# Performance work log

Hardware: AMD Instinct MI355X
Metric: run time of the kernel (lower is better)

## Reference

```python
import jax, jax.numpy as jnp
import numpy as np


def setup_inputs() -> dict:
    key = jax.random.key(0)
    ks = jax.random.split(key, 5)
    B, IN, OUT = 8192, 4096, 4096
    in_q, out_q = IN // 4, OUT // 4
    # xavier-uniform-like scale for weights
    lim = float(np.sqrt(6.0 / (in_q + out_q)))
    return {
        "x": jax.random.normal(ks[0], (B, IN), dtype=jnp.float32),
        "Wa": jax.random.uniform(ks[1], (in_q, out_q), jnp.float32, -lim, lim),
        "Wb": jax.random.uniform(ks[2], (in_q, out_q), jnp.float32, -lim, lim),
        "Wc": jax.random.uniform(ks[3], (in_q, out_q), jnp.float32, -lim, lim),
        "Wd": jax.random.uniform(ks[4], (in_q, out_q), jnp.float32, -lim, lim),
        "bias": jnp.zeros((OUT,), dtype=jnp.float32),
    }


def reference(x, Wa, Wb, Wc, Wd, bias):
    # split quaternion components: [B, in_q] each
    a, b, c, d = jnp.split(x, 4, axis=1)
    # Hamilton product with weight quaternion (right multiplication)
    out_a = a @ Wa - b @ Wb - c @ Wc - d @ Wd
    out_b = a @ Wb + b @ Wa + c @ Wd - d @ Wc
    out_c = a @ Wc - b @ Wd + c @ Wa + d @ Wb
    out_d = a @ Wd + b @ Wc - c @ Wb + d @ Wa
    return jnp.concatenate([out_a, out_b, out_c, out_d], axis=1) + bias
```

## Files before the change

kernel.cpp:

```cpp
#include <hip/hip_runtime.h>
#include <hip/hip_bf16.h>
#include <cstdint>
#include <cstddef>

typedef __bf16 bf16_t;
typedef __bf16 bf16x4 __attribute__((ext_vector_type(4)));
typedef __bf16 bf16x8 __attribute__((ext_vector_type(8)));
typedef float f32x4 __attribute__((ext_vector_type(4)));

#define GLD16(src, dst)                                                       \
    __builtin_amdgcn_global_load_lds(                                         \
        (const __attribute__((address_space(1))) void*)(src),                 \
        (__attribute__((address_space(3))) void*)(dst), 16, 0, 0)

#define BAR() __builtin_amdgcn_s_barrier()
#define WAIT_VM6() asm volatile("s_waitcnt vmcnt(6)" ::: "memory")
#define WAIT_VM0() asm volatile("s_waitcnt vmcnt(0)" ::: "memory")

__global__ __launch_bounds__(256) void cvt_x_kernel(const float* __restrict__ x,
                                                    bf16_t* __restrict__ xb, int n4) {
    int idx = blockIdx.x * blockDim.x + threadIdx.x;
    int stride = gridDim.x * blockDim.x;
    const f32x4* xv = (const f32x4*)x;
    bf16x4* ov = (bf16x4*)xb;
    for (int i = idx; i < n4; i += stride) {
        f32x4 v = xv[i];
        bf16x4 o;
        o[0] = (bf16_t)v[0];
        o[1] = (bf16_t)v[1];
        o[2] = (bf16_t)v[2];
        o[3] = (bf16_t)v[3];
        ov[i] = o;
    }
}

__global__ __launch_bounds__(256) void pack_w_kernel(const float* __restrict__ Wa,
                                                     const float* __restrict__ Wb,
                                                     const float* __restrict__ Wc,
                                                     const float* __restrict__ Wd,
                                                     bf16_t* __restrict__ Mt) {
    __shared__ float tile[64][65];
    const int kb = blockIdx.x * 64;
    const int nb = blockIdx.y * 64;
    const int i = kb >> 10;
    const int j = nb >> 10;

    const float* W[4] = {Wa, Wb, Wc, Wd};
    const int srcIdx[4][4] = {{0, 1, 2, 3}, {1, 0, 3, 2}, {2, 3, 0, 1}, {3, 2, 1, 0}};
    const float sgn[4][4] = {{1.f, 1.f, 1.f, 1.f},
                             {-1.f, 1.f, -1.f, 1.f},
                             {-1.f, 1.f, 1.f, -1.f},
                             {-1.f, -1.f, 1.f, 1.f}};
    const float* Ws = W[srcIdx[i][j]];
    const float s = sgn[i][j];

    const int kq = kb & 1023;
    const int nq = nb & 1023;
    const int tx = threadIdx.x & 63;
    const int ty = threadIdx.x >> 6;

    for (int r = ty; r < 64; r += 4)
        tile[r][tx] = Ws[(size_t)(kq + r) * 1024 + (nq + tx)];
    __syncthreads();
    for (int r = ty; r < 64; r += 4)
        Mt[(size_t)(nb + r) * 4096 + (kb + tx)] = (bf16_t)(s * tile[tx][r]);
}

__global__ __launch_bounds__(512, 2) void qgemm_kernel(const bf16_t* __restrict__ A,
                                                       const bf16_t* __restrict__ Bt,
                                                       const float* __restrict__ bias,
                                                       float* __restrict__ C) {
    constexpr int N = 4096, K = 4096;
    constexpr int NT = K / 64;
    extern __shared__ __align__(16) char lds[];

    const int tid = threadIdx.x;
    const int w = tid >> 6;
    const int lane = tid & 63;
    const int l15 = lane & 15, l4 = lane >> 4;
    const int wr = w >> 2, wc = w & 3;

    const int wg = blockIdx.x;
    const int swz = (wg & 7) * 64 + (wg >> 3);
    const int brow = (swz >> 4) * 256;
    const int bcol = (swz & 15) * 256;

    const int srow = lane >> 3;
    const int skb = (lane & 7) ^ (lane >> 3);

    auto stageA = [&](int buf, int h, int tt) {
#pragma unroll
        for (int q = 0; q < 2; ++q) {
            const bf16_t* src = A + (size_t)(brow + h * 128 + w * 16 + q * 8 + srow) * K +
                                tt * 64 + skb * 8;
            GLD16(src, lds + buf * 32768 + h * 16384 + w * 2048 + q * 1024);
        }
    };
    auto stageB = [&](int buf, int h, int tt) {
#pragma unroll
        for (int q = 0; q < 2; ++q) {
            const bf16_t* src = Bt + (size_t)(bcol + h * 128 + w * 16 + q * 8 + srow) * K +
                                tt * 64 + skb * 8;
            GLD16(src, lds + 65536 + buf * 32768 + h * 16384 + w * 2048 + q * 1024);
        }
    };

    f32x4 acc[8][4] = {};
    bf16x8 a[4][2], b0[2][2], b1[2][2];

    auto ldA = [&](int buf, int mh) {
#pragma unroll
        for (int m = 0; m < 4; ++m)
#pragma unroll
            for (int c = 0; c < 2; ++c)
                a[m][c] = *(const bf16x8*)(lds + buf * 32768 + wr * 16384 +
                                           (mh * 64 + m * 16 + l15) * 128 +
                                           ((c * 4 + l4) ^ (l15 & 7)) * 16);
    };
    auto ldB = [&](int buf, int nh, bf16x8(&b)[2][2]) {
#pragma unroll
        for (int n = 0; n < 2; ++n)
#pragma unroll
            for (int c = 0; c < 2; ++c)
                b[n][c] = *(const bf16x8*)(lds + 65536 + buf * 32768 + (wc >> 1) * 16384 +
                                           ((wc & 1) * 64 + nh * 32 + n * 16 + l15) * 128 +
                                           ((c * 4 + l4) ^ (l15 & 7)) * 16);
    };
    auto mmac = [&](int mh, int nh, bf16x8(&b)[2][2]) {
        __builtin_amdgcn_s_setprio(1);
#pragma unroll
        for (int m = 0; m < 4; ++m)
#pragma unroll
            for (int n = 0; n < 2; ++n)
#pragma unroll
                for (int c = 0; c < 2; ++c)
                    acc[mh * 4 + m][nh * 2 + n] = __builtin_amdgcn_mfma_f32_16x16x32_bf16(
                        a[m][c], b[n][c], acc[mh * 4 + m][nh * 2 + n], 0, 0, 0);
        __builtin_amdgcn_s_setprio(0);
    };

    stageA(0, 0, 0);
    stageA(0, 1, 0);
    stageB(0, 0, 0);
    stageB(0, 1, 0);
    stageB(1, 0, 1);
    stageB(1, 1, 1);
    stageA(1, 0, 1);
    WAIT_VM6();
    BAR();

    for (int tt = 0; tt < NT; ++tt) {
        const int cur = tt & 1;
        ldA(cur, 0);
        ldB(cur, 0, b0);
        if (tt + 1 < NT) stageA(cur ^ 1, 1, tt + 1);
        BAR();
        mmac(0, 0, b0);
        BAR();
        ldB(cur, 1, b1);
        if (tt + 2 < NT) stageB(cur, 0, tt + 2);
        BAR();
        mmac(0, 1, b1);
        BAR();
        ldA(cur, 1);
        if (tt + 2 < NT) stageB(cur, 1, tt + 2);
        BAR();
        mmac(1, 1, b1);
        BAR();
        if (tt + 2 < NT) stageA(cur, 0, tt + 2);
        BAR();
        mmac(1, 0, b0);
        if (tt + 2 < NT) {
            WAIT_VM6();
        } else {
            WAIT_VM0();
        }
        BAR();
    }

#pragma unroll
    for (int n = 0; n < 4; ++n) {
        const int col = bcol + wc * 64 + n * 16 + l15;
        const float bv = bias[col];
#pragma unroll
        for (int m = 0; m < 8; ++m) {
            const int row0 = brow + wr * 128 + m * 16 + l4 * 4;
            const f32x4 v = acc[m][n];
#pragma unroll
            for (int i = 0; i < 4; ++i)
                C[(size_t)(row0 + i) * N + col] = v[i] + bv;
        }
    }
}

extern "C" void kernel_launch(void* const* d_in, const int* in_sizes, int n_in,
                              void* d_out, int out_size, void* d_ws, size_t ws_size,
                              hipStream_t stream) {
    const float* x = (const float*)d_in[0];
    const float* Wa = (const float*)d_in[1];
    const float* Wb = (const float*)d_in[2];
    const float* Wc = (const float*)d_in[3];
    const float* Wd = (const float*)d_in[4];
    const float* bias = (const float*)d_in[5];
    float* out = (float*)d_out;

    const int M = 8192, N = 4096, K = 4096;

    bf16_t* xb = (bf16_t*)d_ws;
    bf16_t* Mt = xb + (size_t)M * K;

    cvt_x_kernel<<<4096, 256, 0, stream>>>(x, xb, (M * K) / 4);
    pack_w_kernel<<<dim3(64, 64), 256, 0, stream>>>(Wa, Wb, Wc, Wd, Mt);

    (void)hipFuncSetAttribute((const void*)qgemm_kernel,
                              hipFuncAttributeMaxDynamicSharedMemorySize, 131072);
    qgemm_kernel<<<dim3((M / 256) * (N / 256)), 512, 131072, stream>>>(xb, Mt, bias, out);
}
```

Measured before the change: 284.6 us.

## Interleave LDS fragment loads with MFMA and prefetch next tile fragments

Splits the A-fragment LDS loads per row-block and moves them between MFMA groups, so LDS reads overlap matrix math instead of sitting behind barriers. The first fragments of the next K-tile are prefetched at the end of each iteration. The vmcnt wait moves earlier and becomes vmcnt(4). B fragments are remapped so each wave reads a 32-column slice from each 128-column half, and the epilogue column mapping changes to match. The price is more live registers and a reordered barrier sequence that has to keep LDS buffer reuse safe.

Result: no change. 285.2 us (+0.2%).

```diff
diff --git a/kernel.cpp b/kernel.cpp
--- a/kernel.cpp
+++ b/kernel.cpp
@@ -13,7 +13,8 @@
         (const __attribute__((address_space(1))) void*)(src),                 \
         (__attribute__((address_space(3))) void*)(dst), 16, 0, 0)
 
-#define BAR() __builtin_amdgcn_s_barrier()
+#define BAR() asm volatile("s_barrier" ::: "memory")
+#define WAIT_VM4() asm volatile("s_waitcnt vmcnt(4)" ::: "memory")
 #define WAIT_VM6() asm volatile("s_waitcnt vmcnt(6)" ::: "memory")
 #define WAIT_VM0() asm volatile("s_waitcnt vmcnt(0)" ::: "memory")
 
@@ -108,22 +109,20 @@
     f32x4 acc[8][4] = {};
     bf16x8 a[4][2], b0[2][2], b1[2][2];
 
-    auto ldA = [&](int buf, int mh) {
-#pragma unroll
-        for (int m = 0; m < 4; ++m)
+    auto ldAm = [&](int buf, int mh, int m) {
+#pragma unroll
+        for (int c = 0; c < 2; ++c)
+            a[m][c] = *(const bf16x8*)(lds + buf * 32768 + wr * 16384 +
+                                       (mh * 64 + m * 16 + l15) * 128 +
+                                       ((c * 4 + l4) ^ (l15 & 7)) * 16);
+    };
+    auto ldB = [&](int buf, int nh, bf16x8(&b)[2][2]) {
+#pragma unroll
+        for (int n = 0; n < 2; ++n)
 #pragma unroll
             for (int c = 0; c < 2; ++c)
-                a[m][c] = *(const bf16x8*)(lds + buf * 32768 + wr * 16384 +
-                                           (mh * 64 + m * 16 + l15) * 128 +
-                                           ((c * 4 + l4) ^ (l15 & 7)) * 16);
-    };
-    auto ldB = [&](int buf, int nh, bf16x8(&b)[2][2]) {
-#pragma unroll
-        for (int n = 0; n < 2; ++n)
-#pragma unroll
-            for (int c = 0; c < 2; ++c)
-                b[n][c] = *(const bf16x8*)(lds + 65536 + buf * 32768 + (wc >> 1) * 16384 +
-                                           ((wc & 1) * 64 + nh * 32 + n * 16 + l15) * 128 +
+                b[n][c] = *(const bf16x8*)(lds + 65536 + buf * 32768 + nh * 16384 +
+                                           (wc * 32 + n * 16 + l15) * 128 +
                                            ((c * 4 + l4) ^ (l15 & 7)) * 16);
     };
     auto mmac = [&](int mh, int nh, bf16x8(&b)[2][2]) {
@@ -148,39 +147,50 @@
     stageA(1, 0, 1);
     WAIT_VM6();
     BAR();
+    ldB(0, 0, b0);
+    ldAm(0, 0, 0);
+    ldAm(0, 0, 1);
 
     for (int tt = 0; tt < NT; ++tt) {
         const int cur = tt & 1;
-        ldA(cur, 0);
-        ldB(cur, 0, b0);
         if (tt + 1 < NT) stageA(cur ^ 1, 1, tt + 1);
         BAR();
+        ldAm(cur, 0, 2);
+        ldAm(cur, 0, 3);
         mmac(0, 0, b0);
-        BAR();
         ldB(cur, 1, b1);
+        BAR();
         if (tt + 2 < NT) stageB(cur, 0, tt + 2);
         BAR();
         mmac(0, 1, b1);
-        BAR();
-        ldA(cur, 1);
+        ldAm(cur, 1, 0);
+        ldAm(cur, 1, 1);
+        BAR();
         if (tt + 2 < NT) stageB(cur, 1, tt + 2);
         BAR();
+        ldAm(cur, 1, 2);
+        ldAm(cur, 1, 3);
         mmac(1, 1, b1);
-        BAR();
-        if (tt + 2 < NT) stageA(cur, 0, tt + 2);
-        BAR();
-        mmac(1, 0, b0);
         if (tt + 2 < NT) {
-            WAIT_VM6();
+            WAIT_VM4();
         } else {
             WAIT_VM0();
         }
         BAR();
+        if (tt + 2 < NT) stageA(cur, 0, tt + 2);
+        BAR();
+        mmac(1, 0, b0);
+        if (tt + 1 < NT) {
+            ldB(cur ^ 1, 0, b0);
+            ldAm(cur ^ 1, 0, 0);
+            ldAm(cur ^ 1, 0, 1);
+        }
+        BAR();
     }
 
 #pragma unroll
     for (int n = 0; n < 4; ++n) {
-        const int col = bcol + wc * 64 + n * 16 + l15;
+        const int col = bcol + (n >> 1) * 128 + wc * 32 + (n & 1) * 16 + l15;
         const float bv = bias[col];
 #pragma unroll
         for (int m = 0; m < 8; ++m) {
```
